# Kernel tuning notes

Measured on AMD Instinct MI355X. Metric: run time of the kernel, lower is better.

The kernel has to match this reference:

```python
import jax, jax.numpy as jnp
import numpy as np

TOPK = 20
N_SAMPLES = 100  # selects_each_sample in the torch code
SQRT2 = 1.4142   # constant used by the torch code


def _normalize(pts):
    # pts: [B,N,3] homogeneous points; weights are all-ones in the torch call path.
    c = pts.mean(axis=1)                                   # [B,3]
    d = pts - c[:, None, :]
    meandist = jnp.sqrt(d[..., 0] ** 2 + d[..., 1] ** 2).mean(axis=1)  # [B]
    s = SQRT2 / meandist
    z = jnp.zeros_like(s)
    o = jnp.ones_like(s)
    T = jnp.stack([
        jnp.stack([s, z, -c[:, 0] * s], axis=-1),
        jnp.stack([z, s, -c[:, 1] * s], axis=-1),
        jnp.stack([z, z, o], axis=-1),
    ], axis=1)                                             # [B,3,3]
    ptsn = jnp.einsum('bij,bnj->bin', T, pts)              # [B,3,N]
    return ptsn, T


def _weighted_svd(pts1, pts2, weights):
    # pts*: [B,N,3], weights: [B,1,N]. Batched (vectorized) version of the
    # per-sample torch.svd loop: smallest right-singular vector of X via eigh
    # of the 9x9 Gram matrix, then rank-2 projection of the 3x3 F via SVD.
    w = weights[:, 0, :, None]                             # [B,N,1]
    p1n, T1 = _normalize(pts1)
    p2n, T2 = _normalize(pts2)
    p = jnp.concatenate([p2n[:, 0:1] * p1n, p2n[:, 1:2] * p1n, p1n], axis=1)  # [B,9,N]
    p = jnp.swapaxes(p, 1, 2)                              # [B,N,9]
    p = p / jnp.linalg.norm(p, axis=2, keepdims=True)      # normalize_SVD=True
    X = p * w                                              # [B,N,9]
    G = jnp.einsum('bni,bnj->bij', X, X)                   # [B,9,9]
    _, evecs = jnp.linalg.eigh(G)
    v = evecs[..., 0]                                      # [B,9] min-eigvec == V[:,-1] of svd(X)
    # canonical sign (torch SVD sign is arbitrary): largest-|.| entry positive
    imax = jnp.argmax(jnp.abs(v), axis=1)
    sgn = jnp.sign(jnp.take_along_axis(v, imax[:, None], axis=1))
    v = v * sgn                                            # unit norm already
    Fm = v.reshape(-1, 3, 3)
    U, S, Vh = jnp.linalg.svd(Fm, full_matrices=False)
    S2 = S * jnp.array([1.0, 1.0, 0.0], dtype=S.dtype)     # mask = [1,1,0]
    F_ = (U * S2[:, None, :]) @ Vh                         # rank-2 projection
    out = jnp.einsum('bji,bjk,bkl->bil', T2, F_, T1)       # T2^T @ F_ @ T1
    residual = jnp.einsum('bni,bi->bn', X, v)              # [B,N]
    return out, residual


def _forward(pts1, pts2, weights, unique_nums, sampled_idx):
    B, N, _ = pts1.shape
    # 1) full weighted 8-point fit
    out, residual = _weighted_svd(pts1, pts2, weights)
    wvec = weights[:, 0, :]                                # [B,N]
    # 2) topK fit over the first `unique_num` entries (masked top_k)
    valid = jnp.arange(N)[None, :] < unique_nums[:, None]
    wm = jnp.where(valid, wvec, -jnp.inf)
    _, idx = jax.lax.top_k(wm, TOPK)                       # [B,20]
    pts1_k = jnp.take_along_axis(pts1, idx[:, :, None], axis=1)
    pts2_k = jnp.take_along_axis(pts2, idx[:, :, None], axis=1)
    w_k = jnp.take_along_axis(wvec, idx, axis=1)[:, None, :]  # [B,1,20]
    out_k, res_k = _weighted_svd(pts1_k, pts2_k, w_k)
    # 3) weighted random subsets (indices precomputed in setup_inputs)
    S_, K_ = sampled_idx.shape[1], sampled_idx.shape[2]
    bidx = jnp.arange(B)[:, None, None]
    p1s = pts1[bidx, sampled_idx]                          # [B,S,K,3]
    p2s = pts2[bidx, sampled_idx]
    ws = wvec[bidx, sampled_idx]                           # [B,S,K]
    w_accu = jnp.prod(ws * 1000.0, axis=2)                 # [B,S]
    w_accu = w_accu / (w_accu.sum(axis=1, keepdims=True) + 1e-10)
    out_s, _ = _weighted_svd(p1s.reshape(B * S_, K_, 3),
                             p2s.reshape(B * S_, K_, 3),
                             ws.reshape(B * S_, 1, K_))
    out_s = out_s.reshape(B, S_, 3, 3)
    return (out, residual, out_k, res_k, out_s, w_accu[..., None])


def setup_inputs() -> dict:
    B, N = 128, 8192
    key = jax.random.key(0)
    k1, k2, k3, k4 = jax.random.split(key, 4)
    pts1 = jax.random.normal(k1, (B, N, 3), dtype=jnp.float32).at[..., 2].set(1.0)
    pts2 = jax.random.normal(k2, (B, N, 3), dtype=jnp.float32).at[..., 2].set(1.0)
    # small positive weights so prod(w*1000, K=20) stays in fp32 range
    weights = jax.random.uniform(k3, (B, 1, N), dtype=jnp.float32) * 0.01 + 1e-6
    un = jax.random.randint(k4, (B,), 1024, N + 1).astype(jnp.int32)
    # per-sample weighted sampling (np.random.choice in the torch code)
    wnp = np.asarray(weights)[:, 0, :].astype(np.float64)
    un_np = np.asarray(un)
    rng = np.random.default_rng(0)
    sampled = np.empty((B, N_SAMPLES, TOPK), np.int32)
    for b in range(B):
        m = int(un_np[b])
        p = wnp[b, :m] / wnp[b, :m].sum()
        sampled[b] = rng.choice(m, size=(N_SAMPLES, TOPK), p=p).astype(np.int32)
    return {"pts1": pts1, "pts2": pts2, "weights": weights,
            "matches_good_unique_nums": un, "sampled_idx": jnp.asarray(sampled)}


def reference(pts1, pts2, weights, matches_good_unique_nums, sampled_idx):
    # returns (out, residual, out_topK, residual_topK,
    #          out_sample_selected_batch, weights_sample_selected_accu_batch)
    return _forward(pts1, pts2, weights, matches_good_unique_nums, sampled_idx)
```

## Files before the change

### kernel.cpp

```cpp
#include <hip/hip_runtime.h>
#include <math.h>

#define NPTS   8192
#define NB     128
#define TOPKN  20
#define NSAMP  100
#define NPROB  (NB + NB + NB * NSAMP)
#define SQRT2C 1.4142

#define OFF_OUT  0
#define OFF_RES  1152
#define OFF_OUTK 1049728
#define OFF_RESK 1050880
#define OFF_OUTS 1053440
#define OFF_WACC 1168640

#define WS_G    0
#define WS_TP   4700160
#define WS_V    5326848
#define WS_TOPK 6266880

__device__ __forceinline__ constexpr int tri9(int i, int j) {
  int a = i < j ? i : j;
  int b = i < j ? j : i;
  return a * 9 - a * (a - 1) / 2 + (b - a);
}

__global__ __launch_bounds__(1024) void prep_kernel(
    const float* __restrict__ pts1, const float* __restrict__ pts2,
    const float* __restrict__ wv, const int* __restrict__ un,
    int* __restrict__ topkidx, double* __restrict__ Gall,
    double* __restrict__ Tpall) {
  __shared__ float sw[NPTS];
  __shared__ float r16a[16], r16b[16], r16c[16], r16d[16];
  __shared__ int   i16[16];
  __shared__ double sred[16][45];
  __shared__ float sbc[6];
  const int tid = threadIdx.x, lane = tid & 63, wid = tid >> 6;

  if (blockIdx.x < NB) {
    const int b = blockIdx.x;
    const int m = un[b];
    const int mlim = (m + 1023) & ~1023;
    for (int n = tid; n < mlim; n += 1024)
      sw[n] = (n < m) ? wv[(size_t)b * NPTS + n] : -INFINITY;
    __syncthreads();
    for (int k = 0; k < TOPKN; ++k) {
      float best = -INFINITY; int bi = 0x7fffffff;
      for (int n = tid; n < mlim; n += 1024) {
        float v = sw[n];
        if (v > best) { best = v; bi = n; }
      }
      #pragma unroll
      for (int off = 32; off > 0; off >>= 1) {
        float ov = __shfl_down(best, off);
        int   oi = __shfl_down(bi, off);
        if (ov > best || (ov == best && oi < bi)) { best = ov; bi = oi; }
      }
      if (lane == 0) { r16a[wid] = best; i16[wid] = bi; }
      __syncthreads();
      if (wid == 0) {
        float v = (lane < 16) ? r16a[lane] : -INFINITY;
        int  ix = (lane < 16) ? i16[lane] : 0x7fffffff;
        #pragma unroll
        for (int off = 8; off > 0; off >>= 1) {
          float ov = __shfl_down(v, off);
          int   oi = __shfl_down(ix, off);
          if (ov > v || (ov == v && oi < ix)) { v = ov; ix = oi; }
        }
        if (lane == 0) { topkidx[b * TOPKN + k] = ix; sw[ix] = -INFINITY; }
      }
      __syncthreads();
    }
    return;
  }

  const int b = blockIdx.x - NB;
  const float* P1 = pts1 + (size_t)b * NPTS * 3;
  const float* P2 = pts2 + (size_t)b * NPTS * 3;
  const float* W  = wv   + (size_t)b * NPTS;

  float x1[8], y1[8], x2[8], y2[8], ww8[8];
  #pragma unroll
  for (int i = 0; i < 8; ++i) {
    const int n = tid + i * 1024;
    x1[i] = P1[n * 3]; y1[i] = P1[n * 3 + 1];
    x2[i] = P2[n * 3]; y2[i] = P2[n * 3 + 1];
    ww8[i] = W[n];
  }

  float sx1 = 0, sy1 = 0, sx2 = 0, sy2 = 0;
  #pragma unroll
  for (int i = 0; i < 8; ++i) { sx1 += x1[i]; sy1 += y1[i]; sx2 += x2[i]; sy2 += y2[i]; }
  #pragma unroll
  for (int off = 32; off > 0; off >>= 1) {
    sx1 += __shfl_down(sx1, off); sy1 += __shfl_down(sy1, off);
    sx2 += __shfl_down(sx2, off); sy2 += __shfl_down(sy2, off);
  }
  if (lane == 0) { r16a[wid] = sx1; r16b[wid] = sy1; r16c[wid] = sx2; r16d[wid] = sy2; }
  __syncthreads();
  if (wid == 0) {
    float a = (lane < 16) ? r16a[lane] : 0.f;
    float bb = (lane < 16) ? r16b[lane] : 0.f;
    float c = (lane < 16) ? r16c[lane] : 0.f;
    float d = (lane < 16) ? r16d[lane] : 0.f;
    #pragma unroll
    for (int off = 8; off > 0; off >>= 1) {
      a += __shfl_down(a, off); bb += __shfl_down(bb, off);
      c += __shfl_down(c, off); d += __shfl_down(d, off);
    }
    if (lane == 0) {
      sbc[0] = a / NPTS; sbc[1] = bb / NPTS; sbc[2] = c / NPTS; sbc[3] = d / NPTS;
    }
  }
  __syncthreads();
  const float cx1 = sbc[0], cy1 = sbc[1], cx2 = sbc[2], cy2 = sbc[3];

  float d1 = 0, d2 = 0;
  #pragma unroll
  for (int i = 0; i < 8; ++i) {
    float ax = x1[i] - cx1, ay = y1[i] - cy1;
    float bx = x2[i] - cx2, by = y2[i] - cy2;
    d1 += sqrtf(ax * ax + ay * ay);
    d2 += sqrtf(bx * bx + by * by);
  }
  #pragma unroll
  for (int off = 32; off > 0; off >>= 1) { d1 += __shfl_down(d1, off); d2 += __shfl_down(d2, off); }
  __syncthreads();
  if (lane == 0) { r16a[wid] = d1; r16b[wid] = d2; }
  __syncthreads();
  if (wid == 0) {
    float a = (lane < 16) ? r16a[lane] : 0.f;
    float bb = (lane < 16) ? r16b[lane] : 0.f;
    #pragma unroll
    for (int off = 8; off > 0; off >>= 1) { a += __shfl_down(a, off); bb += __shfl_down(bb, off); }
    if (lane == 0) {
      sbc[4] = (float)SQRT2C / (a / NPTS);
      sbc[5] = (float)SQRT2C / (bb / NPTS);
    }
  }
  __syncthreads();
  const float s1 = sbc[4], s2 = sbc[5];

  float g[45];
  #pragma unroll
  for (int i = 0; i < 45; ++i) g[i] = 0.f;
  #pragma unroll
  for (int i = 0; i < 8; ++i) {
    float p1x = s1 * (x1[i] - cx1), p1y = s1 * (y1[i] - cy1);
    float p2x = s2 * (x2[i] - cx2), p2y = s2 * (y2[i] - cy2);
    float f[9] = { p2x * p1x, p2x * p1y, p2x,
                   p2y * p1x, p2y * p1y, p2y,
                   p1x, p1y, 1.f };
    float n2 = 0.f;
    #pragma unroll
    for (int j = 0; j < 9; ++j) n2 += f[j] * f[j];
    float sc = ww8[i] / sqrtf(n2);
    #pragma unroll
    for (int j = 0; j < 9; ++j) f[j] *= sc;
    int t = 0;
    #pragma unroll
    for (int a = 0; a < 9; ++a)
      #pragma unroll
      for (int c = a; c < 9; ++c) { g[t] += f[a] * f[c]; ++t; }
  }
  #pragma unroll
  for (int t = 0; t < 45; ++t) {
    float v = g[t];
    #pragma unroll
    for (int off = 32; off > 0; off >>= 1) v += __shfl_down(v, off);
    if (lane == 0) sred[wid][t] = (double)v;
  }
  __syncthreads();
  if (tid < 45) {
    double a = 0;
    #pragma unroll
    for (int w = 0; w < 16; ++w) a += sred[w][tid];
    Gall[(size_t)tid * NPROB + b] = a;
  }
  if (tid == 0) {
    Tpall[0 * NPROB + b] = (double)s1;  Tpall[1 * NPROB + b] = (double)cx1;
    Tpall[2 * NPROB + b] = (double)cy1; Tpall[3 * NPROB + b] = (double)s2;
    Tpall[4 * NPROB + b] = (double)cx2; Tpall[5 * NPROB + b] = (double)cy2;
  }
}

__global__ __launch_bounds__(256) void small_g_kernel(
    const float* __restrict__ pts1, const float* __restrict__ pts2,
    const float* __restrict__ wv, const int* __restrict__ topkidx,
    const int* __restrict__ sampled, double* __restrict__ Gall,
    double* __restrict__ Tpall) {
  const int p = blockIdx.x * blockDim.x + threadIdx.x;
  if (p >= NB + NB * NSAMP) return;
  const int prob = NB + p;
  int b; const int* idx;
  if (p < NB) { b = p; idx = topkidx + p * TOPKN; }
  else { int q = p - NB; b = q / NSAMP; idx = sampled + (size_t)q * TOPKN; }
  const float* P1 = pts1 + (size_t)b * NPTS * 3;
  const float* P2 = pts2 + (size_t)b * NPTS * 3;
  const float* W  = wv   + (size_t)b * NPTS;

  float x1[TOPKN], y1[TOPKN], x2[TOPKN], y2[TOPKN], ww[TOPKN];
  #pragma unroll
  for (int k = 0; k < TOPKN; ++k) {
    int n = idx[k];
    x1[k] = P1[n * 3]; y1[k] = P1[n * 3 + 1];
    x2[k] = P2[n * 3]; y2[k] = P2[n * 3 + 1];
    ww[k] = W[n];
  }
  float cx1 = 0, cy1 = 0, cx2 = 0, cy2 = 0;
  #pragma unroll
  for (int k = 0; k < TOPKN; ++k) { cx1 += x1[k]; cy1 += y1[k]; cx2 += x2[k]; cy2 += y2[k]; }
  cx1 /= TOPKN; cy1 /= TOPKN; cx2 /= TOPKN; cy2 /= TOPKN;
  float d1 = 0, d2 = 0;
  #pragma unroll
  for (int k = 0; k < TOPKN; ++k) {
    float ax = x1[k] - cx1, ay = y1[k] - cy1; d1 += sqrtf(ax * ax + ay * ay);
    float bx = x2[k] - cx2, by = y2[k] - cy2; d2 += sqrtf(bx * bx + by * by);
  }
  const float s1 = (float)SQRT2C / (d1 / TOPKN), s2 = (float)SQRT2C / (d2 / TOPKN);

  float g[45];
  #pragma unroll
  for (int i = 0; i < 45; ++i) g[i] = 0.f;
  #pragma unroll
  for (int k = 0; k < TOPKN; ++k) {
    float p1x = s1 * (x1[k] - cx1), p1y = s1 * (y1[k] - cy1);
    float p2x = s2 * (x2[k] - cx2), p2y = s2 * (y2[k] - cy2);
    float f[9] = { p2x * p1x, p2x * p1y, p2x,
                   p2y * p1x, p2y * p1y, p2y,
                   p1x, p1y, 1.f };
    float n2 = 0.f;
    #pragma unroll
    for (int i = 0; i < 9; ++i) n2 += f[i] * f[i];
    float sc = ww[k] / sqrtf(n2);
    #pragma unroll
    for (int i = 0; i < 9; ++i) f[i] *= sc;
    int t = 0;
    #pragma unroll
    for (int i = 0; i < 9; ++i)
      #pragma unroll
      for (int j = i; j < 9; ++j) { g[t] += f[i] * f[j]; ++t; }
  }
  #pragma unroll
  for (int i = 0; i < 45; ++i) Gall[(size_t)i * NPROB + prob] = (double)g[i];
  Tpall[0 * NPROB + prob] = (double)s1;  Tpall[1 * NPROB + prob] = (double)cx1;
  Tpall[2 * NPROB + prob] = (double)cy1; Tpall[3 * NPROB + prob] = (double)s2;
  Tpall[4 * NPROB + prob] = (double)cx2; Tpall[5 * NPROB + prob] = (double)cy2;
}

__global__ __launch_bounds__(64, 1) void solve_kernel(
    const double* __restrict__ Gall, const double* __restrict__ Tpall,
    double* __restrict__ vall, float* __restrict__ dout) {
  const int prob = blockIdx.x * 64 + threadIdx.x;
  if (prob >= NPROB) return;

  float g[45];
  #pragma unroll
  for (int i = 0; i < 45; ++i) g[i] = (float)Gall[(size_t)i * NPROB + prob];

  float Vf[9][9];
  #pragma unroll
  for (int i = 0; i < 9; ++i)
    #pragma unroll
    for (int j = 0; j < 9; ++j) Vf[i][j] = (i == j) ? 1.0f : 0.0f;

  for (int sweep = 0; sweep < 5; ++sweep) {
    #pragma unroll
    for (int p = 0; p < 9; ++p) {
      #pragma unroll
      for (int q = p + 1; q < 9; ++q) {
        float apq = g[tri9(p, q)];
        if (fabsf(apq) > 1e-30f) {
          float app = g[tri9(p, p)], aqq = g[tri9(q, q)];
          float thf = (aqq - app) * 0.5f * __builtin_amdgcn_rcpf(apq);
          float rr  = __builtin_amdgcn_sqrtf(1.0f + thf * thf);
          float tf  = __builtin_amdgcn_rcpf(fabsf(thf) + rr);
          if (thf < 0.0f) tf = -tf;
          float cf  = __builtin_amdgcn_rsqf(1.0f + tf * tf);
          float sf  = tf * cf;
          float tauf = sf * __builtin_amdgcn_rcpf(1.0f + cf);
          g[tri9(p, p)] = app - tf * apq;
          g[tri9(q, q)] = aqq + tf * apq;
          g[tri9(p, q)] = 0.0f;
          #pragma unroll
          for (int k = 0; k < 9; ++k) {
            if (k != p && k != q) {
              float akp = g[tri9(k, p)], akq = g[tri9(k, q)];
              g[tri9(k, p)] = akp - sf * (akq + tauf * akp);
              g[tri9(k, q)] = akq + sf * (akp - tauf * akq);
            }
          }
          #pragma unroll
          for (int k = 0; k < 9; ++k) {
            float a = Vf[k][p], b2 = Vf[k][q];
            Vf[k][p] = cf * a - sf * b2;
            Vf[k][q] = sf * a + cf * b2;
          }
        }
      }
    }
  }

  int imin = 0; float emin = g[tri9(0, 0)];
  #pragma unroll
  for (int i = 1; i < 9; ++i) {
    float d = g[tri9(i, i)];
    if (d < emin) { emin = d; imin = i; }
  }
  double v[9];
  #pragma unroll
  for (int k = 0; k < 9; ++k) v[k] = (double)Vf[k][0];
  #pragma unroll
  for (int j = 1; j < 9; ++j) {
    bool take = (j == imin);
    #pragma unroll
    for (int k = 0; k < 9; ++k) v[k] = take ? (double)Vf[k][j] : v[k];
  }
  {
    double n2 = 0;
    #pragma unroll
    for (int i = 0; i < 9; ++i) n2 += v[i] * v[i];
    double inv = 1.0 / sqrt(n2);
    #pragma unroll
    for (int i = 0; i < 9; ++i) v[i] *= inv;
  }
  int imax = 0; double amax = fabs(v[0]);
  #pragma unroll
  for (int i = 1; i < 9; ++i) { double a = fabs(v[i]); if (a > amax) { amax = a; imax = i; } }
  double vmax = v[0];
  #pragma unroll
  for (int i = 1; i < 9; ++i) vmax = (i == imax) ? v[i] : vmax;
  double sgn = (vmax > 0.0) ? 1.0 : ((vmax < 0.0) ? -1.0 : 0.0);
  #pragma unroll
  for (int i = 0; i < 9; ++i) v[i] *= sgn;

  #pragma unroll
  for (int i = 0; i < 9; ++i) vall[(size_t)i * NPROB + prob] = v[i];

  double F[3][3] = { { v[0], v[1], v[2] }, { v[3], v[4], v[5] }, { v[6], v[7], v[8] } };
  float M[3][3];
  #pragma unroll
  for (int i = 0; i < 3; ++i)
    #pragma unroll
    for (int j = 0; j < 3; ++j) {
      double acc = 0;
      #pragma unroll
      for (int k = 0; k < 3; ++k) acc += F[k][i] * F[k][j];
      M[i][j] = (float)acc;
    }
  float W3[3][3] = { { 1, 0, 0 }, { 0, 1, 0 }, { 0, 0, 1 } };
  for (int sweep = 0; sweep < 6; ++sweep) {
    #pragma unroll
    for (int p = 0; p < 3; ++p) {
      #pragma unroll
      for (int q = p + 1; q < 3; ++q) {
        float apq = M[p][q];
        if (fabsf(apq) > 1e-30f) {
          float thf = (M[q][q] - M[p][p]) * 0.5f * __builtin_amdgcn_rcpf(apq);
          float rr  = __builtin_amdgcn_sqrtf(1.0f + thf * thf);
          float tf  = __builtin_amdgcn_rcpf(fabsf(thf) + rr);
          if (thf < 0.0f) tf = -tf;
          float cf  = __builtin_amdgcn_rsqf(1.0f + tf * tf);
          float sf  = tf * cf;
          #pragma unroll
          for (int k = 0; k < 3; ++k) {
            float a = M[k][p], bq = M[k][q];
            M[k][p] = cf * a - sf * bq; M[k][q] = sf * a + cf * bq;
          }
          #pragma unroll
          for (int k = 0; k < 3; ++k) {
            float a = M[p][k], bq = M[q][k];
            M[p][k] = cf * a - sf * bq; M[q][k] = sf * a + cf * bq;
          }
          #pragma unroll
          for (int k = 0; k < 3; ++k) {
            float a = W3[k][p], bq = W3[k][q];
            W3[k][p] = cf * a - sf * bq; W3[k][q] = sf * a + cf * bq;
          }
        }
      }
    }
  }
  int i3 = 0; float e3 = M[0][0];
  if (M[1][1] < e3) { e3 = M[1][1]; i3 = 1; }
  if (M[2][2] < e3) { e3 = M[2][2]; i3 = 2; }
  float v3f[3];
  #pragma unroll
  for (int k = 0; k < 3; ++k) v3f[k] = W3[k][0];
  #pragma unroll
  for (int j = 1; j < 3; ++j) {
    bool take = (j == i3);
    #pragma unroll
    for (int k = 0; k < 3; ++k) v3f[k] = take ? W3[k][j] : v3f[k];
  }
  double v3[3] = { (double)v3f[0], (double)v3f[1], (double)v3f[2] };
  {
    double n2 = v3[0]*v3[0] + v3[1]*v3[1] + v3[2]*v3[2];
    double inv = 1.0 / sqrt(n2);
    v3[0] *= inv; v3[1] *= inv; v3[2] *= inv;
  }
  double Fv[3];
  #pragma unroll
  for (int i = 0; i < 3; ++i) Fv[i] = F[i][0] * v3[0] + F[i][1] * v3[1] + F[i][2] * v3[2];
  double Fr[3][3];
  #pragma unroll
  for (int i = 0; i < 3; ++i)
    #pragma unroll
    for (int j = 0; j < 3; ++j) Fr[i][j] = F[i][j] - Fv[i] * v3[j];

  double s1 = Tpall[0 * NPROB + prob], cx1 = Tpall[1 * NPROB + prob], cy1 = Tpall[2 * NPROB + prob];
  double s2 = Tpall[3 * NPROB + prob], cx2 = Tpall[4 * NPROB + prob], cy2 = Tpall[5 * NPROB + prob];
  double B1[3][3];
  #pragma unroll
  for (int i = 0; i < 3; ++i) {
    B1[i][0] = Fr[i][0] * s1;
    B1[i][1] = Fr[i][1] * s1;
    B1[i][2] = -Fr[i][0] * s1 * cx1 - Fr[i][1] * s1 * cy1 + Fr[i][2];
  }
  double O[3][3];
  #pragma unroll
  for (int l = 0; l < 3; ++l) {
    O[0][l] = s2 * B1[0][l];
    O[1][l] = s2 * B1[1][l];
    O[2][l] = -cx2 * s2 * B1[0][l] - cy2 * s2 * B1[1][l] + B1[2][l];
  }
  float* dst;
  if (prob < NB)            dst = dout + OFF_OUT  + prob * 9;
  else if (prob < 2 * NB)   dst = dout + OFF_OUTK + (prob - NB) * 9;
  else                      dst = dout + OFF_OUTS + (size_t)(prob - 2 * NB) * 9;
  #pragma unroll
  for (int i = 0; i < 3; ++i)
    #pragma unroll
    for (int j = 0; j < 3; ++j) dst[i * 3 + j] = (float)O[i][j];
}

__device__ inline double resid_point(double s1, double cx1, double cy1,
                                     double s2, double cx2, double cy2,
                                     float x1, float y1, float x2, float y2,
                                     float w, const double* __restrict__ v) {
  double p1x = s1 * ((double)x1 - cx1), p1y = s1 * ((double)y1 - cy1);
  double p2x = s2 * ((double)x2 - cx2), p2y = s2 * ((double)y2 - cy2);
  double f0 = p2x * p1x, f1 = p2x * p1y, f2 = p2x;
  double f3 = p2y * p1x, f4 = p2y * p1y, f5 = p2y;
  double f6 = p1x, f7 = p1y, f8 = 1.0;
  double n2 = f0 * f0 + f1 * f1 + f2 * f2 + f3 * f3 + f4 * f4 + f5 * f5 +
              f6 * f6 + f7 * f7 + f8 * f8;
  double sc = (double)w / sqrt(n2);
  double dt = f0 * v[0] + f1 * v[1] + f2 * v[2] + f3 * v[3] + f4 * v[4] +
              f5 * v[5] + f6 * v[6] + f7 * v[7] + f8 * v[8];
  return sc * dt;
}

__global__ __launch_bounds__(256) void tail_kernel(
    const float* __restrict__ pts1, const float* __restrict__ pts2,
    const float* __restrict__ wv, const int* __restrict__ topkidx,
    const int* __restrict__ sampled, const double* __restrict__ Tpall,
    const double* __restrict__ vall, float* __restrict__ dout) {
  const int bid = blockIdx.x, tid = threadIdx.x;
  if (bid < NB * (NPTS / 256)) {
    const int b = bid >> 5;
    const int n = (bid & 31) * 256 + tid;
    double Tp[6], v[9];
    #pragma unroll
    for (int j = 0; j < 6; ++j) Tp[j] = Tpall[(size_t)j * NPROB + b];
    #pragma unroll
    for (int j = 0; j < 9; ++j) v[j] = vall[(size_t)j * NPROB + b];
    const float* P1 = pts1 + ((size_t)b * NPTS + n) * 3;
    const float* P2 = pts2 + ((size_t)b * NPTS + n) * 3;
    float w = wv[(size_t)b * NPTS + n];
    double r = resid_point(Tp[0], Tp[1], Tp[2], Tp[3], Tp[4], Tp[5],
                           P1[0], P1[1], P2[0], P2[1], w, v);
    dout[OFF_RES + (size_t)b * NPTS + n] = (float)r;
    return;
  }
  const int b = bid - NB * (NPTS / 256);
  if (tid < TOPKN) {
    const int prob = NB + b;
    double Tp[6], v[9];
    #pragma unroll
    for (int j = 0; j < 6; ++j) Tp[j] = Tpall[(size_t)j * NPROB + prob];
    #pragma unroll
    for (int j = 0; j < 9; ++j) v[j] = vall[(size_t)j * NPROB + prob];
    int n = topkidx[b * TOPKN + tid];
    const float* P1 = pts1 + ((size_t)b * NPTS + n) * 3;
    const float* P2 = pts2 + ((size_t)b * NPTS + n) * 3;
    float w = wv[(size_t)b * NPTS + n];
    double r = resid_point(Tp[0], Tp[1], Tp[2], Tp[3], Tp[4], Tp[5],
                           P1[0], P1[1], P2[0], P2[1], w, v);
    dout[OFF_RESK + b * TOPKN + tid] = (float)r;
  }
  __shared__ double ssum[256];
  double prod = 0.0;
  if (tid < NSAMP) {
    const int* idx = sampled + ((size_t)b * NSAMP + tid) * TOPKN;
    prod = 1.0;
    #pragma unroll
    for (int k = 0; k < TOPKN; ++k)
      prod *= (double)wv[(size_t)b * NPTS + idx[k]] * 1000.0;
  }
  ssum[tid] = prod;
  __syncthreads();
  for (int off = 128; off > 0; off >>= 1) {
    if (tid < off) ssum[tid] += ssum[tid + off];
    __syncthreads();
  }
  double tot = ssum[0];
  if (tid < NSAMP) dout[OFF_WACC + b * NSAMP + tid] = (float)(prod / (tot + 1e-10));
}

extern "C" void kernel_launch(void* const* d_in, const int* in_sizes, int n_in,
                              void* d_out, int out_size, void* d_ws, size_t ws_size,
                              hipStream_t stream) {
  const float* pts1   = (const float*)d_in[0];
  const float* pts2   = (const float*)d_in[1];
  const float* wv     = (const float*)d_in[2];
  const int* un       = (const int*)d_in[3];
  const int* sampled  = (const int*)d_in[4];
  float* dout = (float*)d_out;
  char* ws = (char*)d_ws;
  double* Gall   = (double*)(ws + WS_G);
  double* Tpall  = (double*)(ws + WS_TP);
  double* vall   = (double*)(ws + WS_V);
  int*    topkix = (int*)(ws + WS_TOPK);

  prep_kernel<<<2 * NB, 1024, 0, stream>>>(pts1, pts2, wv, un, topkix, Gall, Tpall);
  small_g_kernel<<<(NB + NB * NSAMP + 255) / 256, 256, 0, stream>>>(
      pts1, pts2, wv, topkix, sampled, Gall, Tpall);
  solve_kernel<<<(NPROB + 63) / 64, 64, 0, stream>>>(Gall, Tpall, vall, dout);
  tail_kernel<<<NB * (NPTS / 256) + NB, 256, 0, stream>>>(
      pts1, pts2, wv, topkix, sampled, Tpall, vall, dout);
}
```

Measured before the change: 184.0 us.

## Fold sampled-subset Gram computation into prep kernel to overlap with top-k

The Gram and normalization work for the 12800 sampled subsets now runs in extra blocks of the prep kernel, since it does not depend on the top-k selection. Only the 128 top-k subsets stay in a separate tiny one-block kernel that runs after prep. The goal is to overlap the sampled Gram work with the serial top-k and full-set reductions and to shorten the dependent launch chain. In exchange, the sampled work now runs in 1024-thread blocks under prep's launch bounds and shared-memory allocation, which can cap registers and occupancy for the register-heavy gram20 code.

```diff
diff --git a/kernel.cpp b/kernel.cpp
--- a/kernel.cpp
+++ b/kernel.cpp
@@ -26,17 +26,88 @@
   return a * 9 - a * (a - 1) / 2 + (b - a);
 }
 
+__device__ __forceinline__ void gram20(
+    const float* __restrict__ pts1, const float* __restrict__ pts2,
+    const float* __restrict__ wv, int b, const int* __restrict__ idx,
+    int prob, double* __restrict__ Gall, double* __restrict__ Tpall) {
+  const float* P1 = pts1 + (size_t)b * NPTS * 3;
+  const float* P2 = pts2 + (size_t)b * NPTS * 3;
+  const float* W  = wv   + (size_t)b * NPTS;
+
+  float x1[TOPKN], y1[TOPKN], x2[TOPKN], y2[TOPKN], ww[TOPKN];
+  #pragma unroll
+  for (int k = 0; k < TOPKN; ++k) {
+    int n = idx[k];
+    x1[k] = P1[n * 3]; y1[k] = P1[n * 3 + 1];
+    x2[k] = P2[n * 3]; y2[k] = P2[n * 3 + 1];
+    ww[k] = W[n];
+  }
+  float cx1 = 0, cy1 = 0, cx2 = 0, cy2 = 0;
+  #pragma unroll
+  for (int k = 0; k < TOPKN; ++k) { cx1 += x1[k]; cy1 += y1[k]; cx2 += x2[k]; cy2 += y2[k]; }
+  cx1 /= TOPKN; cy1 /= TOPKN; cx2 /= TOPKN; cy2 /= TOPKN;
+  float d1 = 0, d2 = 0;
+  #pragma unroll
+  for (int k = 0; k < TOPKN; ++k) {
+    float ax = x1[k] - cx1, ay = y1[k] - cy1; d1 += sqrtf(ax * ax + ay * ay);
+    float bx = x2[k] - cx2, by = y2[k] - cy2; d2 += sqrtf(bx * bx + by * by);
+  }
+  const float s1 = (float)SQRT2C / (d1 / TOPKN), s2 = (float)SQRT2C / (d2 / TOPKN);
+
+  float g[45];
+  #pragma unroll
+  for (int i = 0; i < 45; ++i) g[i] = 0.f;
+  #pragma unroll
+  for (int k = 0; k < TOPKN; ++k) {
+    float p1x = s1 * (x1[k] - cx1), p1y = s1 * (y1[k] - cy1);
+    float p2x = s2 * (x2[k] - cx2), p2y = s2 * (y2[k] - cy2);
+    float f[9] = { p2x * p1x, p2x * p1y, p2x,
+                   p2y * p1x, p2y * p1y, p2y,
+                   p1x, p1y, 1.f };
+    float n2 = 0.f;
+    #pragma unroll
+    for (int i = 0; i < 9; ++i) n2 += f[i] * f[i];
+    float sc = ww[k] / sqrtf(n2);
+    #pragma unroll
+    for (int i = 0; i < 9; ++i) f[i] *= sc;
+    int t = 0;
+    #pragma unroll
+    for (int i = 0; i < 9; ++i)
+      #pragma unroll
+      for (int j = i; j < 9; ++j) { g[t] += f[i] * f[j]; ++t; }
+  }
+  #pragma unroll
+  for (int i = 0; i < 45; ++i) Gall[(size_t)i * NPROB + prob] = (double)g[i];
+  Tpall[0 * NPROB + prob] = (double)s1;  Tpall[1 * NPROB + prob] = (double)cx1;
+  Tpall[2 * NPROB + prob] = (double)cy1; Tpall[3 * NPROB + prob] = (double)s2;
+  Tpall[4 * NPROB + prob] = (double)cx2; Tpall[5 * NPROB + prob] = (double)cy2;
+}
+
+#define SAMP_BLK0 256
+#define NBLK_PREP 269
 __global__ __launch_bounds__(1024) void prep_kernel(
     const float* __restrict__ pts1, const float* __restrict__ pts2,
     const float* __restrict__ wv, const int* __restrict__ un,
+    const int* __restrict__ sampled,
     int* __restrict__ topkidx, double* __restrict__ Gall,
     double* __restrict__ Tpall) {
+  const int tid = threadIdx.x, lane = tid & 63, wid = tid >> 6;
+
+  if (blockIdx.x >= SAMP_BLK0) {
+    const int p = (blockIdx.x - SAMP_BLK0) * 1024 + tid;
+    if (p < NB * NSAMP) {
+      const int b = p / NSAMP;
+      gram20(pts1, pts2, wv, b, sampled + (size_t)p * TOPKN,
+             2 * NB + p, Gall, Tpall);
+    }
+    return;
+  }
+
   __shared__ float sw[NPTS];
   __shared__ float r16a[16], r16b[16], r16c[16], r16d[16];
   __shared__ int   i16[16];
   __shared__ double sred[16][45];
   __shared__ float sbc[6];
-  const int tid = threadIdx.x, lane = tid & 63, wid = tid >> 6;
 
   if (blockIdx.x < NB) {
     const int b = blockIdx.x;
@@ -185,68 +256,13 @@
   }
 }
 
-__global__ __launch_bounds__(256) void small_g_kernel(
+__global__ __launch_bounds__(128) void topk_gram_kernel(
     const float* __restrict__ pts1, const float* __restrict__ pts2,
     const float* __restrict__ wv, const int* __restrict__ topkidx,
-    const int* __restrict__ sampled, double* __restrict__ Gall,
-    double* __restrict__ Tpall) {
-  const int p = blockIdx.x * blockDim.x + threadIdx.x;
-  if (p >= NB + NB * NSAMP) return;
-  const int prob = NB + p;
-  int b; const int* idx;
-  if (p < NB) { b = p; idx = topkidx + p * TOPKN; }
-  else { int q = p - NB; b = q / NSAMP; idx = sampled + (size_t)q * TOPKN; }
-  const float* P1 = pts1 + (size_t)b * NPTS * 3;
-  const float* P2 = pts2 + (size_t)b * NPTS * 3;
-  const float* W  = wv   + (size_t)b * NPTS;
-
-  float x1[TOPKN], y1[TOPKN], x2[TOPKN], y2[TOPKN], ww[TOPKN];
-  #pragma unroll
-  for (int k = 0; k < TOPKN; ++k) {
-    int n = idx[k];
-    x1[k] = P1[n * 3]; y1[k] = P1[n * 3 + 1];
-    x2[k] = P2[n * 3]; y2[k] = P2[n * 3 + 1];
-    ww[k] = W[n];
-  }
-  float cx1 = 0, cy1 = 0, cx2 = 0, cy2 = 0;
-  #pragma unroll
-  for (int k = 0; k < TOPKN; ++k) { cx1 += x1[k]; cy1 += y1[k]; cx2 += x2[k]; cy2 += y2[k]; }
-  cx1 /= TOPKN; cy1 /= TOPKN; cx2 /= TOPKN; cy2 /= TOPKN;
-  float d1 = 0, d2 = 0;
-  #pragma unroll
-  for (int k = 0; k < TOPKN; ++k) {
-    float ax = x1[k] - cx1, ay = y1[k] - cy1; d1 += sqrtf(ax * ax + ay * ay);
-    float bx = x2[k] - cx2, by = y2[k] - cy2; d2 += sqrtf(bx * bx + by * by);
-  }
-  const float s1 = (float)SQRT2C / (d1 / TOPKN), s2 = (float)SQRT2C / (d2 / TOPKN);
-
-  float g[45];
-  #pragma unroll
-  for (int i = 0; i < 45; ++i) g[i] = 0.f;
-  #pragma unroll
-  for (int k = 0; k < TOPKN; ++k) {
-    float p1x = s1 * (x1[k] - cx1), p1y = s1 * (y1[k] - cy1);
-    float p2x = s2 * (x2[k] - cx2), p2y = s2 * (y2[k] - cy2);
-    float f[9] = { p2x * p1x, p2x * p1y, p2x,
-                   p2y * p1x, p2y * p1y, p2y,
-                   p1x, p1y, 1.f };
-    float n2 = 0.f;
-    #pragma unroll
-    for (int i = 0; i < 9; ++i) n2 += f[i] * f[i];
-    float sc = ww[k] / sqrtf(n2);
-    #pragma unroll
-    for (int i = 0; i < 9; ++i) f[i] *= sc;
-    int t = 0;
-    #pragma unroll
-    for (int i = 0; i < 9; ++i)
-      #pragma unroll
-      for (int j = i; j < 9; ++j) { g[t] += f[i] * f[j]; ++t; }
-  }
-  #pragma unroll
-  for (int i = 0; i < 45; ++i) Gall[(size_t)i * NPROB + prob] = (double)g[i];
-  Tpall[0 * NPROB + prob] = (double)s1;  Tpall[1 * NPROB + prob] = (double)cx1;
-  Tpall[2 * NPROB + prob] = (double)cy1; Tpall[3 * NPROB + prob] = (double)s2;
-  Tpall[4 * NPROB + prob] = (double)cx2; Tpall[5 * NPROB + prob] = (double)cy2;
+    double* __restrict__ Gall, double* __restrict__ Tpall) {
+  const int p = threadIdx.x;
+  if (p < NB)
+    gram20(pts1, pts2, wv, p, topkidx + p * TOPKN, NB + p, Gall, Tpall);
 }
 
 __global__ __launch_bounds__(64, 1) void solve_kernel(
@@ -524,9 +540,9 @@
   double* vall   = (double*)(ws + WS_V);
   int*    topkix = (int*)(ws + WS_TOPK);
 
-  prep_kernel<<<2 * NB, 1024, 0, stream>>>(pts1, pts2, wv, un, topkix, Gall, Tpall);
-  small_g_kernel<<<(NB + NB * NSAMP + 255) / 256, 256, 0, stream>>>(
-      pts1, pts2, wv, topkix, sampled, Gall, Tpall);
+  prep_kernel<<<NBLK_PREP, 1024, 0, stream>>>(pts1, pts2, wv, un, sampled,
+                                              topkix, Gall, Tpall);
+  topk_gram_kernel<<<1, 128, 0, stream>>>(pts1, pts2, wv, topkix, Gall, Tpall);
   solve_kernel<<<(NPROB + 63) / 64, 64, 0, stream>>>(Gall, Tpall, vall, dout);
   tail_kernel<<<NB * (NPTS / 256) + NB, 256, 0, stream>>>(
       pts1, pts2, wv, topkix, sampled, Tpall, vall, dout);
```

Measured after the change: 247.5 us. 34.5% more time.
